# Optimization experiments

Measured on AMD Instinct MI355X. Metric: run time of the kernel, lower is better.

The kernel has to match this reference:

```python
import jax, jax.numpy as jnp
import numpy as np

N = 50000      # nodes
E = 800000     # edges (avg degree 16)
G = 512        # graphs in batch
F_IN = 14      # raw atom features
D = 64         # hidden feats_dim after projection
M = 64         # m_dim
L = 3          # egnn layers

silu = jax.nn.silu


def setup_inputs() -> dict:
    key = jax.random.key(0)
    ks = jax.random.split(key, 32)
    s = 0.1  # weight scale
    def w(k, shape):
        return jax.random.normal(k, shape, dtype=jnp.float32) * s
    inp = {
        "x": jax.random.normal(ks[0], (N, F_IN), dtype=jnp.float32),
        "pos": jax.random.normal(ks[1], (N, 3), dtype=jnp.float32),
        "edge_index": jax.random.randint(ks[2], (2, E), 0, N, dtype=jnp.int32),
        "batch": jnp.sort(jax.random.randint(ks[3], (N,), 0, G, dtype=jnp.int32)),
        # feat projection 14 -> 64
        "proj_w": w(ks[4], (F_IN, D)), "proj_b": jnp.zeros((D,), jnp.float32),
        # per-layer EGNN params, stacked over L layers
        "edge_w1": w(ks[5], (L, 2 * D, M)), "edge_b1": jnp.zeros((L, M), jnp.float32),
        "edge_w2": w(ks[6], (L, M, M)),     "edge_b2": jnp.zeros((L, M), jnp.float32),
        "node_w1": w(ks[7], (L, D + M, M)), "node_b1": jnp.zeros((L, M), jnp.float32),
        "node_w2": w(ks[8], (L, M, D)),     "node_b2": jnp.zeros((L, D), jnp.float32),
        # readout head
        "lin1_w": w(ks[9], (D, M)),  "lin1_b": jnp.zeros((M,), jnp.float32),
        "lin2_w": w(ks[10], (M, D)), "lin2_b": jnp.zeros((D,), jnp.float32),
        "lin3_w": w(ks[11], (D, M)), "lin3_b": jnp.zeros((M,), jnp.float32),
        "lin4_w": w(ks[12], (M, 1)), "lin4_b": jnp.zeros((1,), jnp.float32),
    }
    return inp


def reference(x, pos, edge_index, batch,
              proj_w, proj_b,
              edge_w1, edge_b1, edge_w2, edge_b2,
              node_w1, node_b1, node_w2, node_b2,
              lin1_w, lin1_b, lin2_w, lin2_b, lin3_w, lin3_b, lin4_w, lin4_b):
    # feature projection (do_feat_proj since dim > num_feat)
    h = x @ proj_w + proj_b                         # [N, D]
    src, dst = edge_index[0], edge_index[1]          # x_j = source, x_i = target
    for l in range(L):
        # message: edge_mlp(concat(x_i, x_j))
        cat = jnp.concatenate([h[dst], h[src]], axis=-1)       # [E, 2D]
        m = silu(cat @ edge_w1[l] + edge_b1[l])                 # [E, M]
        m = silu(m @ edge_w2[l] + edge_b2[l])                   # [E, M]
        # aggregate: scatter-add to target nodes
        agg = jax.ops.segment_sum(m, dst, num_segments=N)       # [N, M]
        # node update: node_mlp(concat(x, m_i)) + x
        u = jnp.concatenate([h, agg], axis=-1)                  # [N, D+M]
        u = silu(u @ node_w1[l] + node_b1[l])
        h = u @ node_w2[l] + node_b2[l] + h                      # residual
    per_atom_out = h                                             # [N, D]
    o = silu(h @ lin1_w + lin1_b) @ lin2_w + lin2_b              # [N, D]
    o = jax.ops.segment_sum(o, batch, num_segments=G)            # [G, D]
    o = silu(o @ lin3_w + lin3_b) @ lin4_w + lin4_b              # [G, 1]
    return o.reshape(-1), per_atom_out
```

## Files before the change

kernel.cpp:

```cpp
#include <hip/hip_runtime.h>

#define NN 50000
#define EE 800000
#define GG 512
#define LL 3

typedef short bf16x8 __attribute__((ext_vector_type(8)));
typedef float f32x4  __attribute__((ext_vector_type(4)));

__device__ __forceinline__ float silu_f(float x) {
    return x * __builtin_amdgcn_rcpf(1.0f + __expf(-x));
}
__device__ __forceinline__ unsigned short bf16_rne(float x) {
    unsigned u = __float_as_uint(x);
    u += 0x7fffu + ((u >> 16) & 1u);
    return (unsigned short)(u >> 16);
}
__device__ __forceinline__ float bflo(unsigned u) { return __uint_as_float(u << 16); }
__device__ __forceinline__ float bfhi(unsigned u) { return __uint_as_float(u & 0xffff0000u); }
__device__ __forceinline__ f32x4 mfma16(bf16x8 a, bf16x8 b, f32x4 c) {
    return __builtin_amdgcn_mfma_f32_16x16x32_bf16(a, b, c, 0, 0, 0);
}
__device__ __forceinline__ void barrier_lgkm() {
    asm volatile("s_waitcnt lgkmcnt(0)" ::: "memory");
    __builtin_amdgcn_s_barrier();
}

__global__ __launch_bounds__(256) void hist_kernel(const int* __restrict__ ei,
                                                   int* __restrict__ deg) {
    int e = blockIdx.x * 256 + threadIdx.x;
    if (e < EE) atomicAdd(&deg[ei[EE + e]], 1);
}

__global__ __launch_bounds__(512) void scanA_kernel(const int* __restrict__ deg,
                                                    int* __restrict__ rowptr,
                                                    int* __restrict__ bsum) {
    __shared__ int wsum[8];
    const int tid = threadIdx.x, b = blockIdx.x;
    int i = b * 512 + tid;
    int v = (i < NN) ? deg[i] : 0;
    int lane = tid & 63, wid = tid >> 6;
    int x = v;
#pragma unroll
    for (int s = 1; s < 64; s <<= 1) {
        int u = __shfl_up(x, s, 64);
        if (lane >= s) x += u;
    }
    if (lane == 63) wsum[wid] = x;
    __syncthreads();
    int woff = 0;
    for (int w = 0; w < wid; ++w) woff += wsum[w];
    if (i < NN) rowptr[i] = woff + x - v;
    if (tid == 511) bsum[b] = woff + x;
}

__global__ __launch_bounds__(128) void scanB_kernel(int* __restrict__ bsum, int nb) {
    __shared__ int wsum[2];
    const int tid = threadIdx.x;
    int v = (tid < nb) ? bsum[tid] : 0;
    int lane = tid & 63, wid = tid >> 6;
    int x = v;
#pragma unroll
    for (int s = 1; s < 64; s <<= 1) {
        int u = __shfl_up(x, s, 64);
        if (lane >= s) x += u;
    }
    if (lane == 63) wsum[wid] = x;
    __syncthreads();
    int woff = (wid == 1) ? wsum[0] : 0;
    if (tid < nb) bsum[tid] = woff + x - v;
}

__global__ __launch_bounds__(512) void scanC_kernel(int* __restrict__ rowptr,
                                                    int* __restrict__ cursor,
                                                    const int* __restrict__ bsum) {
    const int tid = threadIdx.x, b = blockIdx.x;
    int i = b * 512 + tid;
    if (i < NN) {
        int r = rowptr[i] + bsum[b];
        rowptr[i] = r;
        cursor[i] = r;
    }
    if (i == 0) rowptr[NN] = EE;
}

__global__ __launch_bounds__(256) void scatter_kernel(const int* __restrict__ ei,
                                                      int* __restrict__ cursor,
                                                      int* __restrict__ srcsS,
                                                      int* __restrict__ dstsS) {
    int e = blockIdx.x * 256 + threadIdx.x;
    if (e < EE) {
        int d = ei[EE + e];
        int pos = atomicAdd(&cursor[d], 1);
        srcsS[pos] = ei[e];
        dstsS[pos] = d;
    }
}

__global__ __launch_bounds__(512, 4) void pk_kernel(
    const float* __restrict__ h, const float* __restrict__ w1g,
    float* __restrict__ Pt, unsigned short* __restrict__ Pbu, int ntiles)
{
    extern __shared__ float lds[];
    float* ws = lds;
    float* hs = ws + 8192;
    const int tid = threadIdx.x;
    const int tr  = tid & 31;
    const int tc  = tid >> 5;

    for (int i = tid; i < 2048; i += 512)
        *(float4*)&ws[4 * i] = *(const float4*)&w1g[4 * i];

    for (int tile = blockIdx.x; tile < ntiles; tile += gridDim.x) {
        const int base = tile * 128;
        __syncthreads();
#pragma unroll
        for (int rep = 0; rep < 4; ++rep) {
            int idx = rep * 512 + tid;
            int r = idx >> 4, q = idx & 15;
            int n = base + r;
            float4 v = make_float4(0.f, 0.f, 0.f, 0.f);
            if (n < NN) v = *(const float4*)(h + 64 * n + 4 * q);
            *(float4*)&hs[r * 68 + 4 * q] = v;
        }
        __syncthreads();
#pragma unroll
        for (int p = 0; p < 2; ++p) {
            float acc[4][4];
#pragma unroll
            for (int jj = 0; jj < 4; ++jj)
#pragma unroll
                for (int ii = 0; ii < 4; ++ii) acc[jj][ii] = 0.f;
#pragma unroll 4
            for (int k16 = 0; k16 < 16; ++k16) {
                float4 bv0 = *(const float4*)&ws[(p * 64 + 4 * k16 + 0) * 64 + 4 * tc];
                float4 bv1 = *(const float4*)&ws[(p * 64 + 4 * k16 + 1) * 64 + 4 * tc];
                float4 bv2 = *(const float4*)&ws[(p * 64 + 4 * k16 + 2) * 64 + 4 * tc];
                float4 bv3 = *(const float4*)&ws[(p * 64 + 4 * k16 + 3) * 64 + 4 * tc];
#pragma unroll
                for (int jj = 0; jj < 4; ++jj) {
                    float4 av = *(const float4*)&hs[(tr + 32 * jj) * 68 + 4 * k16];
                    acc[jj][0] = fmaf(av.x, bv0.x, fmaf(av.y, bv1.x, fmaf(av.z, bv2.x, fmaf(av.w, bv3.x, acc[jj][0]))));
                    acc[jj][1] = fmaf(av.x, bv0.y, fmaf(av.y, bv1.y, fmaf(av.z, bv2.y, fmaf(av.w, bv3.y, acc[jj][1]))));
                    acc[jj][2] = fmaf(av.x, bv0.z, fmaf(av.y, bv1.z, fmaf(av.z, bv2.z, fmaf(av.w, bv3.z, acc[jj][2]))));
                    acc[jj][3] = fmaf(av.x, bv0.w, fmaf(av.y, bv1.w, fmaf(av.z, bv2.w, fmaf(av.w, bv3.w, acc[jj][3]))));
                }
            }
#pragma unroll
            for (int jj = 0; jj < 4; ++jj) {
                int n = base + tr + 32 * jj;
                if (n < NN) {
                    if (p == 0) {
                        *(float4*)(Pt + (size_t)64 * n + 4 * tc) =
                            make_float4(acc[jj][0], acc[jj][1], acc[jj][2], acc[jj][3]);
                    } else {
                        uint2 o;
                        o.x = ((unsigned)bf16_rne(acc[jj][1]) << 16) | bf16_rne(acc[jj][0]);
                        o.y = ((unsigned)bf16_rne(acc[jj][3]) << 16) | bf16_rne(acc[jj][2]);
                        *(uint2*)(Pbu + (size_t)64 * n + 4 * tc) = o;
                    }
                }
            }
        }
    }
}

__global__ __launch_bounds__(512, 6) void edge_kernel(
    const float* __restrict__ Pt, const unsigned short* __restrict__ Pbu,
    const int* __restrict__ srcsS, const int* __restrict__ dstsS,
    const float* __restrict__ b1g,
    const float* __restrict__ w2g, const float* __restrict__ b2g,
    unsigned short* __restrict__ m2g, int ntiles)
{
    extern __shared__ __align__(16) char smem[];
    char*  wt2s = smem;
    char*  m1s  = wt2s + 8192;
    float* b1s  = (float*)(m1s + 16384);
    float* b2s  = b1s + 64;

    const int tid = threadIdx.x;
    const int l   = tid & 63;
    const int w   = tid >> 6;
    const int mi  = w >> 1;
    const int ni  = w & 1;
    const int l15 = l & 15;
    const int l4  = l >> 4;
    const int g7  = tid & 7;

    {
        int c = tid >> 3, kc = tid & 7;
        const float* wp = w2g + (kc * 8) * 64 + c;
        bf16x8 bv;
#pragma unroll
        for (int j = 0; j < 8; ++j) bv[j] = (short)bf16_rne(wp[j * 64]);
        *(bf16x8*)(wt2s + c * 128 + ((kc * 16) ^ ((c & 7) << 4))) = bv;
    }
    if (tid < 64) { b1s[tid] = b1g[tid]; b2s[tid] = b2g[tid]; }

    int    ix_d[2], ix_s[2];
    float4 pf_a0[2], pf_a1[2];
    uint4  pf_pb[2];

    auto IDX = [&](int tt) {
        int eb = tt * 128;
#pragma unroll
        for (int it = 0; it < 2; ++it) {
            int e = (it * 512 + tid) >> 3;
            ix_d[it] = dstsS[eb + e];
            ix_s[it] = srcsS[eb + e];
        }
    };
    auto DATA = [&]() {
#pragma unroll
        for (int it = 0; it < 2; ++it) {
            const float* pt = Pt + (size_t)64 * ix_d[it] + 8 * g7;
            pf_a0[it] = *(const float4*)pt;
            pf_a1[it] = *(const float4*)(pt + 4);
            pf_pb[it] = *(const uint4*)(Pbu + (size_t)64 * ix_s[it] + 8 * g7);
        }
    };

    int tile = blockIdx.x;
    if (tile < ntiles) { IDX(tile); DATA(); }
    if (tile + gridDim.x < ntiles) IDX(tile + gridDim.x);
    barrier_lgkm();

    for (; tile < ntiles; tile += gridDim.x) {
#pragma unroll
        for (int it = 0; it < 2; ++it) {
            int e = (it * 512 + tid) >> 3;
            float4 b0  = *(const float4*)(b1s + 8 * g7);
            float4 b1v = *(const float4*)(b1s + 8 * g7 + 4);
            float v0 = silu_f(pf_a0[it].x + bflo(pf_pb[it].x) + b0.x);
            float v1 = silu_f(pf_a0[it].y + bfhi(pf_pb[it].x) + b0.y);
            float v2 = silu_f(pf_a0[it].z + bflo(pf_pb[it].y) + b0.z);
            float v3 = silu_f(pf_a0[it].w + bfhi(pf_pb[it].y) + b0.w);
            float v4 = silu_f(pf_a1[it].x + bflo(pf_pb[it].z) + b1v.x);
            float v5 = silu_f(pf_a1[it].y + bfhi(pf_pb[it].z) + b1v.y);
            float v6 = silu_f(pf_a1[it].z + bflo(pf_pb[it].w) + b1v.z);
            float v7 = silu_f(pf_a1[it].w + bfhi(pf_pb[it].w) + b1v.w);
            uint4 o;
            o.x = ((unsigned)bf16_rne(v1) << 16) | bf16_rne(v0);
            o.y = ((unsigned)bf16_rne(v3) << 16) | bf16_rne(v2);
            o.z = ((unsigned)bf16_rne(v5) << 16) | bf16_rne(v4);
            o.w = ((unsigned)bf16_rne(v7) << 16) | bf16_rne(v6);
            *(uint4*)(m1s + e * 128 + ((g7 * 16) ^ ((e & 7) << 4))) = o;
        }
        barrier_lgkm();
        int nxt = tile + gridDim.x;
        if (nxt < ntiles) {
            DATA();
            if (nxt + gridDim.x < ntiles) IDX(nxt + gridDim.x);
        }
        f32x4 acc2[2][2];
#pragma unroll
        for (int m = 0; m < 2; ++m)
#pragma unroll
            for (int n = 0; n < 2; ++n) {
                float b = b2s[32 * ni + 16 * n + l15];
                acc2[m][n] = (f32x4){b, b, b, b};
            }
        const int sw = (l15 & 7) << 4;
#pragma unroll
        for (int ks = 0; ks < 2; ++ks) {
            int kb = ks * 64 + l4 * 16;
            bf16x8 af[2], bfr[2];
#pragma unroll
            for (int m = 0; m < 2; ++m)
                af[m] = *(const bf16x8*)(m1s + (32 * mi + 16 * m + l15) * 128 + (kb ^ sw));
#pragma unroll
            for (int n = 0; n < 2; ++n)
                bfr[n] = *(const bf16x8*)(wt2s + (32 * ni + 16 * n + l15) * 128 + (kb ^ sw));
#pragma unroll
            for (int m = 0; m < 2; ++m)
#pragma unroll
                for (int n = 0; n < 2; ++n)
                    acc2[m][n] = mfma16(af[m], bfr[n], acc2[m][n]);
        }
        unsigned short* mg = m2g + (size_t)(tile * 128) * 64;
#pragma unroll
        for (int m = 0; m < 2; ++m)
#pragma unroll
            for (int n = 0; n < 2; ++n)
#pragma unroll
                for (int r = 0; r < 4; ++r) {
                    int row = 32 * mi + 16 * m + l4 * 4 + r;
                    int col = 32 * ni + 16 * n + l15;
                    mg[row * 64 + col] = bf16_rne(silu_f(acc2[m][n][r]));
                }
        barrier_lgkm();
    }
}

__global__ __launch_bounds__(256) void agg_kernel(
    const unsigned short* __restrict__ m2g, const int* __restrict__ rowptr,
    float* __restrict__ agg)
{
    int idx = blockIdx.x * 256 + threadIdx.x;
    if (idx >= NN * 16) return;
    int n = idx >> 4, c = idx & 15;
    int e0 = rowptr[n], e1 = rowptr[n + 1];
    float a0 = 0.f, a1 = 0.f, a2 = 0.f, a3 = 0.f;
    int e = e0;
    for (; e + 4 <= e1; e += 4) {
        uint2 u0 = *(const uint2*)(m2g + (size_t)(e + 0) * 64 + 4 * c);
        uint2 u1 = *(const uint2*)(m2g + (size_t)(e + 1) * 64 + 4 * c);
        uint2 u2 = *(const uint2*)(m2g + (size_t)(e + 2) * 64 + 4 * c);
        uint2 u3 = *(const uint2*)(m2g + (size_t)(e + 3) * 64 + 4 * c);
        a0 += (bflo(u0.x) + bflo(u1.x)) + (bflo(u2.x) + bflo(u3.x));
        a1 += (bfhi(u0.x) + bfhi(u1.x)) + (bfhi(u2.x) + bfhi(u3.x));
        a2 += (bflo(u0.y) + bflo(u1.y)) + (bflo(u2.y) + bflo(u3.y));
        a3 += (bfhi(u0.y) + bfhi(u1.y)) + (bfhi(u2.y) + bfhi(u3.y));
    }
    for (; e < e1; ++e) {
        uint2 u = *(const uint2*)(m2g + (size_t)e * 64 + 4 * c);
        a0 += bflo(u.x); a1 += bfhi(u.x);
        a2 += bflo(u.y); a3 += bfhi(u.y);
    }
    *(float4*)(agg + (size_t)64 * n + 4 * c) = make_float4(a0, a1, a2, a3);
}

__global__ __launch_bounds__(512, 1) void node_mlp_kernel(
    const float* __restrict__ A, const float* __restrict__ A2,
    const float* __restrict__ w1g, const float* __restrict__ b1g,
    const float* __restrict__ w2g, const float* __restrict__ b2g,
    float* __restrict__ outp, int nrows, int ntiles)
{
    extern __shared__ float lds[];
    float* ws1  = lds;
    float* ws2  = ws1 + 8192;
    float* wb1  = ws2 + 4096;
    float* wb2  = wb1 + 64;
    float* cats = wb2 + 64;
    float* m1s  = cats + 128 * 132;

    const int tid = threadIdx.x;
    const int tr  = tid & 31;
    const int tc  = tid >> 5;

    for (int i = tid; i < 2048; i += 512)
        *(float4*)&ws1[4 * i] = *(const float4*)&w1g[4 * i];
    for (int i = tid; i < 1024; i += 512)
        *(float4*)&ws2[4 * i] = *(const float4*)&w2g[4 * i];
    if (tid < 64) { wb1[tid] = b1g[tid]; wb2[tid] = b2g[tid]; }

    for (int tile = blockIdx.x; tile < ntiles; tile += gridDim.x) {
        const int base = tile * 128;
        __syncthreads();
#pragma unroll
        for (int rep = 0; rep < 8; ++rep) {
            int idx = rep * 512 + tid;
            int r = idx >> 5, q = idx & 31;
            int n = base + r;
            float4 v = make_float4(0.f, 0.f, 0.f, 0.f);
            if (n < nrows)
                v = (q < 16) ? *(const float4*)(A + 64 * n + 4 * q)
                             : *(const float4*)(A2 + 64 * n + 4 * (q - 16));
            *(float4*)&cats[r * 132 + 4 * q] = v;
        }
        __syncthreads();
        float acc[4][4];
#pragma unroll
        for (int jj = 0; jj < 4; ++jj)
#pragma unroll
            for (int ii = 0; ii < 4; ++ii) acc[jj][ii] = wb1[4 * tc + ii];
#pragma unroll 4
        for (int k16 = 0; k16 < 32; ++k16) {
            float4 bv0 = *(const float4*)&ws1[(4 * k16 + 0) * 64 + 4 * tc];
            float4 bv1 = *(const float4*)&ws1[(4 * k16 + 1) * 64 + 4 * tc];
            float4 bv2 = *(const float4*)&ws1[(4 * k16 + 2) * 64 + 4 * tc];
            float4 bv3 = *(const float4*)&ws1[(4 * k16 + 3) * 64 + 4 * tc];
#pragma unroll
            for (int jj = 0; jj < 4; ++jj) {
                float4 av = *(const float4*)&cats[(tr + 32 * jj) * 132 + 4 * k16];
                acc[jj][0] = fmaf(av.x, bv0.x, fmaf(av.y, bv1.x, fmaf(av.z, bv2.x, fmaf(av.w, bv3.x, acc[jj][0]))));
                acc[jj][1] = fmaf(av.x, bv0.y, fmaf(av.y, bv1.y, fmaf(av.z, bv2.y, fmaf(av.w, bv3.y, acc[jj][1]))));
                acc[jj][2] = fmaf(av.x, bv0.z, fmaf(av.y, bv1.z, fmaf(av.z, bv2.z, fmaf(av.w, bv3.z, acc[jj][2]))));
                acc[jj][3] = fmaf(av.x, bv0.w, fmaf(av.y, bv1.w, fmaf(av.z, bv2.w, fmaf(av.w, bv3.w, acc[jj][3]))));
            }
        }
#pragma unroll
        for (int jj = 0; jj < 4; ++jj) {
            float4 v;
            v.x = silu_f(acc[jj][0]); v.y = silu_f(acc[jj][1]);
            v.z = silu_f(acc[jj][2]); v.w = silu_f(acc[jj][3]);
            *(float4*)&m1s[(tr + 32 * jj) * 68 + 4 * tc] = v;
        }
        __syncthreads();
        float acc2[4][4];
#pragma unroll
        for (int jj = 0; jj < 4; ++jj)
#pragma unroll
            for (int ii = 0; ii < 4; ++ii) acc2[jj][ii] = wb2[4 * tc + ii];
#pragma unroll 4
        for (int k16 = 0; k16 < 16; ++k16) {
            float4 bv0 = *(const float4*)&ws2[(4 * k16 + 0) * 64 + 4 * tc];
            float4 bv1 = *(const float4*)&ws2[(4 * k16 + 1) * 64 + 4 * tc];
            float4 bv2 = *(const float4*)&ws2[(4 * k16 + 2) * 64 + 4 * tc];
            float4 bv3 = *(const float4*)&ws2[(4 * k16 + 3) * 64 + 4 * tc];
#pragma unroll
            for (int jj = 0; jj < 4; ++jj) {
                float4 av = *(const float4*)&m1s[(tr + 32 * jj) * 68 + 4 * k16];
                acc2[jj][0] = fmaf(av.x, bv0.x, fmaf(av.y, bv1.x, fmaf(av.z, bv2.x, fmaf(av.w, bv3.x, acc2[jj][0]))));
                acc2[jj][1] = fmaf(av.x, bv0.y, fmaf(av.y, bv1.y, fmaf(av.z, bv2.y, fmaf(av.w, bv3.y, acc2[jj][1]))));
                acc2[jj][2] = fmaf(av.x, bv0.z, fmaf(av.y, bv1.z, fmaf(av.z, bv2.z, fmaf(av.w, bv3.z, acc2[jj][2]))));
                acc2[jj][3] = fmaf(av.x, bv0.w, fmaf(av.y, bv1.w, fmaf(av.z, bv2.w, fmaf(av.w, bv3.w, acc2[jj][3]))));
            }
        }
#pragma unroll
        for (int jj = 0; jj < 4; ++jj) {
            int r = tr + 32 * jj;
            int n = base + r;
            if (n < nrows) {
                float4 hold = *(const float4*)&cats[r * 132 + 4 * tc];
                *(float4*)&outp[64 * n + 4 * tc] = make_float4(
                    acc2[jj][0] + hold.x, acc2[jj][1] + hold.y,
                    acc2[jj][2] + hold.z, acc2[jj][3] + hold.w);
            }
        }
    }
}

__global__ __launch_bounds__(512, 1) void rowmlp_ro_kernel(
    const float* __restrict__ A,
    const float* __restrict__ w1g, const float* __restrict__ b1g,
    const float* __restrict__ w2g, const float* __restrict__ b2g,
    const int* __restrict__ seg, float* __restrict__ outp,
    int nrows, int ntiles)
{
    extern __shared__ float lds[];
    float* ws1  = lds;
    float* ws2  = ws1 + 4096;
    float* wb1  = ws2 + 4096;
    float* wb2  = wb1 + 64;
    float* cats = wb2 + 64;
    float* m1s  = cats + 128 * 68;
    int*   segs = (int*)(m1s + 128 * 68);

    const int tid = threadIdx.x;
    const int tr  = tid & 31;
    const int tc  = tid >> 5;

    for (int i = tid; i < 1024; i += 512) {
        *(float4*)&ws1[4 * i] = *(const float4*)&w1g[4 * i];
        *(float4*)&ws2[4 * i] = *(const float4*)&w2g[4 * i];
    }
    if (tid < 64) { wb1[tid] = b1g[tid]; wb2[tid] = b2g[tid]; }

    for (int tile = blockIdx.x; tile < ntiles; tile += gridDim.x) {
        const int base = tile * 128;
        __syncthreads();
        if (tid < 128) segs[tid] = (base + tid < nrows) ? seg[base + tid] : -1;
#pragma unroll
        for (int rep = 0; rep < 4; ++rep) {
            int idx = rep * 512 + tid;
            int r = idx >> 4, q = idx & 15;
            int n = base + r;
            float4 v = make_float4(0.f, 0.f, 0.f, 0.f);
            if (n < nrows) v = *(const float4*)(A + 64 * n + 4 * q);
            *(float4*)&cats[r * 68 + 4 * q] = v;
        }
        __syncthreads();
        float acc[4][4];
#pragma unroll
        for (int jj = 0; jj < 4; ++jj)
#pragma unroll
            for (int ii = 0; ii < 4; ++ii) acc[jj][ii] = wb1[4 * tc + ii];
#pragma unroll 4
        for (int k16 = 0; k16 < 16; ++k16) {
            float4 bv0 = *(const float4*)&ws1[(4 * k16 + 0) * 64 + 4 * tc];
            float4 bv1 = *(const float4*)&ws1[(4 * k16 + 1) * 64 + 4 * tc];
            float4 bv2 = *(const float4*)&ws1[(4 * k16 + 2) * 64 + 4 * tc];
            float4 bv3 = *(const float4*)&ws1[(4 * k16 + 3) * 64 + 4 * tc];
#pragma unroll
            for (int jj = 0; jj < 4; ++jj) {
                float4 av = *(const float4*)&cats[(tr + 32 * jj) * 68 + 4 * k16];
                acc[jj][0] = fmaf(av.x, bv0.x, fmaf(av.y, bv1.x, fmaf(av.z, bv2.x, fmaf(av.w, bv3.x, acc[jj][0]))));
                acc[jj][1] = fmaf(av.x, bv0.y, fmaf(av.y, bv1.y, fmaf(av.z, bv2.y, fmaf(av.w, bv3.y, acc[jj][1]))));
                acc[jj][2] = fmaf(av.x, bv0.z, fmaf(av.y, bv1.z, fmaf(av.z, bv2.z, fmaf(av.w, bv3.z, acc[jj][2]))));
                acc[jj][3] = fmaf(av.x, bv0.w, fmaf(av.y, bv1.w, fmaf(av.z, bv2.w, fmaf(av.w, bv3.w, acc[jj][3]))));
            }
        }
#pragma unroll
        for (int jj = 0; jj < 4; ++jj) {
            float4 v;
            v.x = silu_f(acc[jj][0]); v.y = silu_f(acc[jj][1]);
            v.z = silu_f(acc[jj][2]); v.w = silu_f(acc[jj][3]);
            *(float4*)&m1s[(tr + 32 * jj) * 68 + 4 * tc] = v;
        }
        __syncthreads();
        float acc2[4][4];
#pragma unroll
        for (int jj = 0; jj < 4; ++jj)
#pragma unroll
            for (int ii = 0; ii < 4; ++ii) acc2[jj][ii] = wb2[4 * tc + ii];
#pragma unroll 4
        for (int k16 = 0; k16 < 16; ++k16) {
            float4 bv0 = *(const float4*)&ws2[(4 * k16 + 0) * 64 + 4 * tc];
            float4 bv1 = *(const float4*)&ws2[(4 * k16 + 1) * 64 + 4 * tc];
            float4 bv2 = *(const float4*)&ws2[(4 * k16 + 2) * 64 + 4 * tc];
            float4 bv3 = *(const float4*)&ws2[(4 * k16 + 3) * 64 + 4 * tc];
#pragma unroll
            for (int jj = 0; jj < 4; ++jj) {
                float4 av = *(const float4*)&m1s[(tr + 32 * jj) * 68 + 4 * k16];
                acc2[jj][0] = fmaf(av.x, bv0.x, fmaf(av.y, bv1.x, fmaf(av.z, bv2.x, fmaf(av.w, bv3.x, acc2[jj][0]))));
                acc2[jj][1] = fmaf(av.x, bv0.y, fmaf(av.y, bv1.y, fmaf(av.z, bv2.y, fmaf(av.w, bv3.y, acc2[jj][1]))));
                acc2[jj][2] = fmaf(av.x, bv0.z, fmaf(av.y, bv1.z, fmaf(av.z, bv2.z, fmaf(av.w, bv3.z, acc2[jj][2]))));
                acc2[jj][3] = fmaf(av.x, bv0.w, fmaf(av.y, bv1.w, fmaf(av.z, bv2.w, fmaf(av.w, bv3.w, acc2[jj][3]))));
            }
        }
#pragma unroll
        for (int jj = 0; jj < 4; ++jj) {
            int r = tr + 32 * jj;
            int n = base + r;
            int gid = segs[r];
            float4 vv = (n < nrows) ? make_float4(acc2[jj][0], acc2[jj][1], acc2[jj][2], acc2[jj][3])
                                    : make_float4(0.f, 0.f, 0.f, 0.f);
            unsigned f = (tr == 0 || segs[(r > 0) ? r - 1 : 0] != gid) ? 1u : 0u;
#pragma unroll
            for (int s = 1; s < 32; s <<= 1) {
                float ux = __shfl_up(vv.x, s, 32);
                float uy = __shfl_up(vv.y, s, 32);
                float uz = __shfl_up(vv.z, s, 32);
                float uw = __shfl_up(vv.w, s, 32);
                unsigned uf = __shfl_up(f, s, 32);
                if (tr >= s) {
                    if (!f) { vv.x += ux; vv.y += uy; vv.z += uz; vv.w += uw; }
                    f |= uf;
                }
            }
            bool tail = (tr == 31) || (segs[r + 1] != gid);
            if (tail && gid >= 0) {
                float* bp = outp + 64 * gid + 4 * tc;
                atomicAdd(bp + 0, vv.x); atomicAdd(bp + 1, vv.y);
                atomicAdd(bp + 2, vv.z); atomicAdd(bp + 3, vv.w);
            }
        }
    }
}

__global__ __launch_bounds__(256) void proj_kernel(
    const float* __restrict__ x, const float* __restrict__ w,
    const float* __restrict__ b, float* __restrict__ h, int n)
{
    int i = blockIdx.x * 256 + threadIdx.x;
    if (i >= n * 64) return;
    int node = i >> 6, j = i & 63;
    const float* xr = x + node * 14;
    float acc = b[j];
#pragma unroll
    for (int k = 0; k < 14; ++k) acc = fmaf(xr[k], w[k * 64 + j], acc);
    h[i] = acc;
}

__global__ __launch_bounds__(256) void head_kernel(
    const float* __restrict__ gsum,
    const float* __restrict__ w3, const float* __restrict__ b3,
    const float* __restrict__ w4, const float* __restrict__ b4,
    float* __restrict__ out, int g_count)
{
    int wid  = (blockIdx.x * 256 + threadIdx.x) >> 6;
    int lane = threadIdx.x & 63;
    if (wid >= g_count) return;
    float v = gsum[wid * 64 + lane];
    float t = b3[lane];
#pragma unroll
    for (int k = 0; k < 64; ++k) {
        float a = __shfl(v, k, 64);
        t = fmaf(a, w3[k * 64 + lane], t);
    }
    t = silu_f(t);
    float r = t * w4[lane];
#pragma unroll
    for (int off = 32; off; off >>= 1) r += __shfl_down(r, off, 64);
    if (lane == 0) out[wid] = r + b4[0];
}

extern "C" void kernel_launch(void* const* d_in, const int* in_sizes, int n_in,
                              void* d_out, int out_size, void* d_ws, size_t ws_size,
                              hipStream_t stream)
{
    const float* x      = (const float*)d_in[0];
    const int*   ei     = (const int*)d_in[2];
    const int*   batch  = (const int*)d_in[3];
    const float* proj_w = (const float*)d_in[4];
    const float* proj_b = (const float*)d_in[5];
    const float* ew1 = (const float*)d_in[6];
    const float* eb1 = (const float*)d_in[7];
    const float* ew2 = (const float*)d_in[8];
    const float* eb2 = (const float*)d_in[9];
    const float* nw1 = (const float*)d_in[10];
    const float* nb1 = (const float*)d_in[11];
    const float* nw2 = (const float*)d_in[12];
    const float* nb2 = (const float*)d_in[13];
    const float* l1w = (const float*)d_in[14]; const float* l1b = (const float*)d_in[15];
    const float* l2w = (const float*)d_in[16]; const float* l2b = (const float*)d_in[17];
    const float* l3w = (const float*)d_in[18]; const float* l3b = (const float*)d_in[19];
    const float* l4w = (const float*)d_in[20]; const float* l4b = (const float*)d_in[21];

    float* out  = (float*)d_out;
    float* h    = out + GG;

    unsigned short* m2g = (unsigned short*)d_ws;
    float* gsum = (float*)(m2g + (size_t)EE * 64);
    float* Pt   = gsum + (size_t)GG * 64;
    unsigned short* Pbu = (unsigned short*)(Pt + (size_t)NN * 64);
    int* deg    = (int*)(Pbu + (size_t)NN * 64);
    int* rowptr = deg + NN;
    int* cursor = rowptr + NN + 1;
    int* srcsS  = cursor + NN;
    int* dstsS  = srcsS + EE;
    int* bsum   = dstsS + EE;
    float* agg  = Pt;

    const size_t edge_lds = 8192 + 16384 + 256 + 256;
    const size_t pk_lds   = (size_t)(8192 + 8704) * 4;
    const size_t node_lds = (size_t)(8192 + 4096 + 128 + 128 * 132 + 128 * 68) * 4;
    const size_t ro_lds   = (size_t)(4096 + 4096 + 128 + 128 * 68 + 128 * 68) * 4 + 128 * 4;

    (void)hipFuncSetAttribute((const void*)edge_kernel,
                              hipFuncAttributeMaxDynamicSharedMemorySize, (int)edge_lds);
    (void)hipFuncSetAttribute((const void*)pk_kernel,
                              hipFuncAttributeMaxDynamicSharedMemorySize, (int)pk_lds);
    (void)hipFuncSetAttribute((const void*)node_mlp_kernel,
                              hipFuncAttributeMaxDynamicSharedMemorySize, (int)node_lds);
    (void)hipFuncSetAttribute((const void*)rowmlp_ro_kernel,
                              hipFuncAttributeMaxDynamicSharedMemorySize, (int)ro_lds);

    const int nb = (NN + 511) / 512;
    hipMemsetAsync(deg, 0, (size_t)NN * sizeof(int), stream);
    hipMemsetAsync(gsum, 0, (size_t)GG * 64 * sizeof(float), stream);
    hist_kernel<<<(EE + 255) / 256, 256, 0, stream>>>(ei, deg);
    scanA_kernel<<<nb, 512, 0, stream>>>(deg, rowptr, bsum);
    scanB_kernel<<<1, 128, 0, stream>>>(bsum, nb);
    scanC_kernel<<<nb, 512, 0, stream>>>(rowptr, cursor, bsum);
    scatter_kernel<<<(EE + 255) / 256, 256, 0, stream>>>(ei, cursor, srcsS, dstsS);

    proj_kernel<<<(NN * 64 + 255) / 256, 256, 0, stream>>>(x, proj_w, proj_b, h, NN);

    const int etiles = EE / 128;
    const int ntiles = (NN + 127) / 128;
    for (int l = 0; l < LL; ++l) {
        pk_kernel<<<ntiles, 512, pk_lds, stream>>>(h, ew1 + l * 8192, Pt, Pbu, ntiles);
        edge_kernel<<<1024, 512, edge_lds, stream>>>(
            Pt, Pbu, srcsS, dstsS, eb1 + l * 64, ew2 + l * 4096, eb2 + l * 64,
            m2g, etiles);
        agg_kernel<<<(NN * 16 + 255) / 256, 256, 0, stream>>>(m2g, rowptr, agg);
        node_mlp_kernel<<<196, 512, node_lds, stream>>>(
            h, agg, nw1 + l * 8192, nb1 + l * 64, nw2 + l * 4096, nb2 + l * 64,
            h, NN, ntiles);
    }
    rowmlp_ro_kernel<<<196, 512, ro_lds, stream>>>(
        h, l1w, l1b, l2w, l2b, batch, gsum, NN, ntiles);
    head_kernel<<<GG / 4, 256, 0, stream>>>(gsum, l3w, l3b, l4w, l4b, out, GG);
}
```

Before: 511.3 us.

## Fuse segment-sum aggregation into edge kernel via LDS segmented reduction

```diff
diff --git a/kernel.cpp b/kernel.cpp
--- a/kernel.cpp
+++ b/kernel.cpp
@@ -165,18 +165,20 @@
     }
 }
 
-__global__ __launch_bounds__(512, 6) void edge_kernel(
+__global__ __launch_bounds__(512, 4) void edge_kernel(
     const float* __restrict__ Pt, const unsigned short* __restrict__ Pbu,
     const int* __restrict__ srcsS, const int* __restrict__ dstsS,
     const float* __restrict__ b1g,
     const float* __restrict__ w2g, const float* __restrict__ b2g,
-    unsigned short* __restrict__ m2g, int ntiles)
+    float* __restrict__ agg, int ntiles)
 {
     extern __shared__ __align__(16) char smem[];
-    char*  wt2s = smem;
-    char*  m1s  = wt2s + 8192;
-    float* b1s  = (float*)(m1s + 16384);
-    float* b2s  = b1s + 64;
+    char*  wt2s  = smem;
+    char*  m1s   = wt2s + 8192;
+    char*  m2h   = m1s + 16384;
+    float* b1s   = (float*)(m2h + 17408);
+    float* b2s   = b1s + 64;
+    int*   dstsL = (int*)(b2s + 64);
 
     const int tid = threadIdx.x;
     const int l   = tid & 63;
@@ -197,9 +199,10 @@
     }
     if (tid < 64) { b1s[tid] = b1g[tid]; b2s[tid] = b2g[tid]; }
 
-    int    ix_d[2], ix_s[2];
+    int    ix_d[2], ix_s[2], ix_pd = 0;
     float4 pf_a0[2], pf_a1[2];
     uint4  pf_pb[2];
+    int    pf_d = 0;
 
     auto IDX = [&](int tt) {
         int eb = tt * 128;
@@ -209,6 +212,7 @@
             ix_d[it] = dstsS[eb + e];
             ix_s[it] = srcsS[eb + e];
         }
+        ix_pd = (tid < 128) ? dstsS[eb + tid] : 0;
     };
     auto DATA = [&]() {
 #pragma unroll
@@ -218,14 +222,17 @@
             pf_a1[it] = *(const float4*)(pt + 4);
             pf_pb[it] = *(const uint4*)(Pbu + (size_t)64 * ix_s[it] + 8 * g7);
         }
+        pf_d = ix_pd;
     };
 
     int tile = blockIdx.x;
+    int buf  = 0;
     if (tile < ntiles) { IDX(tile); DATA(); }
     if (tile + gridDim.x < ntiles) IDX(tile + gridDim.x);
     barrier_lgkm();
 
     for (; tile < ntiles; tile += gridDim.x) {
+        if (tid < 128) dstsL[buf * 128 + tid] = pf_d;
 #pragma unroll
         for (int it = 0; it < 2; ++it) {
             int e = (it * 512 + tid) >> 3;
@@ -277,7 +284,6 @@
                 for (int n = 0; n < 2; ++n)
                     acc2[m][n] = mfma16(af[m], bfr[n], acc2[m][n]);
         }
-        unsigned short* mg = m2g + (size_t)(tile * 128) * 64;
 #pragma unroll
         for (int m = 0; m < 2; ++m)
 #pragma unroll
@@ -286,38 +292,51 @@
                 for (int r = 0; r < 4; ++r) {
                     int row = 32 * mi + 16 * m + l4 * 4 + r;
                     int col = 32 * ni + 16 * n + l15;
-                    mg[row * 64 + col] = bf16_rne(silu_f(acc2[m][n][r]));
+                    *(unsigned short*)(m2h + row * 136 + col * 2) =
+                        bf16_rne(silu_f(acc2[m][n][r]));
                 }
         barrier_lgkm();
-    }
-}
-
-__global__ __launch_bounds__(256) void agg_kernel(
-    const unsigned short* __restrict__ m2g, const int* __restrict__ rowptr,
-    float* __restrict__ agg)
-{
-    int idx = blockIdx.x * 256 + threadIdx.x;
-    if (idx >= NN * 16) return;
-    int n = idx >> 4, c = idx & 15;
-    int e0 = rowptr[n], e1 = rowptr[n + 1];
-    float a0 = 0.f, a1 = 0.f, a2 = 0.f, a3 = 0.f;
-    int e = e0;
-    for (; e + 4 <= e1; e += 4) {
-        uint2 u0 = *(const uint2*)(m2g + (size_t)(e + 0) * 64 + 4 * c);
-        uint2 u1 = *(const uint2*)(m2g + (size_t)(e + 1) * 64 + 4 * c);
-        uint2 u2 = *(const uint2*)(m2g + (size_t)(e + 2) * 64 + 4 * c);
-        uint2 u3 = *(const uint2*)(m2g + (size_t)(e + 3) * 64 + 4 * c);
-        a0 += (bflo(u0.x) + bflo(u1.x)) + (bflo(u2.x) + bflo(u3.x));
-        a1 += (bfhi(u0.x) + bfhi(u1.x)) + (bfhi(u2.x) + bfhi(u3.x));
-        a2 += (bflo(u0.y) + bflo(u1.y)) + (bflo(u2.y) + bflo(u3.y));
-        a3 += (bfhi(u0.y) + bfhi(u1.y)) + (bfhi(u2.y) + bfhi(u3.y));
-    }
-    for (; e < e1; ++e) {
-        uint2 u = *(const uint2*)(m2g + (size_t)e * 64 + 4 * c);
-        a0 += bflo(u.x); a1 += bfhi(u.x);
-        a2 += bflo(u.y); a3 += bfhi(u.y);
-    }
-    *(float4*)(agg + (size_t)64 * n + 4 * c) = make_float4(a0, a1, a2, a3);
+        {
+            const int* dL = dstsL + buf * 128;
+            int r  = tid & 127;
+            int cg = tid >> 7;
+            int d  = dL[r];
+            bool head = (r == 0) || (dL[r - 1] != d);
+            if (head) {
+                float s[16];
+#pragma unroll
+                for (int j = 0; j < 16; ++j) s[j] = 0.f;
+                int rr = r;
+                do {
+                    const char* p = m2h + rr * 136 + cg * 32;
+                    uint2 u0 = *(const uint2*)(p);
+                    uint2 u1 = *(const uint2*)(p + 8);
+                    uint2 u2 = *(const uint2*)(p + 16);
+                    uint2 u3 = *(const uint2*)(p + 24);
+                    s[0]  += bflo(u0.x); s[1]  += bfhi(u0.x);
+                    s[2]  += bflo(u0.y); s[3]  += bfhi(u0.y);
+                    s[4]  += bflo(u1.x); s[5]  += bfhi(u1.x);
+                    s[6]  += bflo(u1.y); s[7]  += bfhi(u1.y);
+                    s[8]  += bflo(u2.x); s[9]  += bfhi(u2.x);
+                    s[10] += bflo(u2.y); s[11] += bfhi(u2.y);
+                    s[12] += bflo(u3.x); s[13] += bfhi(u3.x);
+                    s[14] += bflo(u3.y); s[15] += bfhi(u3.y);
+                    ++rr;
+                } while (rr < 128 && dL[rr] == d);
+                float* ap = agg + (size_t)64 * d + cg * 16;
+                if (r > 0 && rr < 128) {
+                    *(float4*)(ap + 0)  = make_float4(s[0], s[1], s[2], s[3]);
+                    *(float4*)(ap + 4)  = make_float4(s[4], s[5], s[6], s[7]);
+                    *(float4*)(ap + 8)  = make_float4(s[8], s[9], s[10], s[11]);
+                    *(float4*)(ap + 12) = make_float4(s[12], s[13], s[14], s[15]);
+                } else {
+#pragma unroll
+                    for (int j = 0; j < 16; ++j) atomicAdd(ap + j, s[j]);
+                }
+            }
+        }
+        buf ^= 1;
+    }
 }
 
 __global__ __launch_bounds__(512, 1) void node_mlp_kernel(
@@ -601,8 +620,8 @@
     float* out  = (float*)d_out;
     float* h    = out + GG;
 
-    unsigned short* m2g = (unsigned short*)d_ws;
-    float* gsum = (float*)(m2g + (size_t)EE * 64);
+    float* agg  = (float*)d_ws;
+    float* gsum = agg + (size_t)NN * 64;
     float* Pt   = gsum + (size_t)GG * 64;
     unsigned short* Pbu = (unsigned short*)(Pt + (size_t)NN * 64);
     int* deg    = (int*)(Pbu + (size_t)NN * 64);
@@ -611,9 +630,8 @@
     int* srcsS  = cursor + NN;
     int* dstsS  = srcsS + EE;
     int* bsum   = dstsS + EE;
-    float* agg  = Pt;
-
-    const size_t edge_lds = 8192 + 16384 + 256 + 256;
+
+    const size_t edge_lds = 8192 + 16384 + 17408 + 256 + 256 + 1024;
     const size_t pk_lds   = (size_t)(8192 + 8704) * 4;
     const size_t node_lds = (size_t)(8192 + 4096 + 128 + 128 * 132 + 128 * 68) * 4;
     const size_t ro_lds   = (size_t)(4096 + 4096 + 128 + 128 * 68 + 128 * 68) * 4 + 128 * 4;
@@ -642,10 +660,10 @@
     const int ntiles = (NN + 127) / 128;
     for (int l = 0; l < LL; ++l) {
         pk_kernel<<<ntiles, 512, pk_lds, stream>>>(h, ew1 + l * 8192, Pt, Pbu, ntiles);
-        edge_kernel<<<1024, 512, edge_lds, stream>>>(
+        hipMemsetAsync(agg, 0, (size_t)NN * 64 * sizeof(float), stream);
+        edge_kernel<<<768, 512, edge_lds, stream>>>(
             Pt, Pbu, srcsS, dstsS, eb1 + l * 64, ew2 + l * 4096, eb2 + l * 64,
-            m2g, etiles);
-        agg_kernel<<<(NN * 16 + 255) / 256, 256, 0, stream>>>(m2g, rowptr, agg);
+            agg, etiles);
         node_mlp_kernel<<<196, 512, node_lds, stream>>>(
             h, agg, nw1 + l * 8192, nb1 + l * 64, nw2 + l * 4096, nb2 + l * 64,
             h, NN, ntiles);
```

Result: slower. 719.3 us (+40.7%).

## Rewrite per-node projection kernel with bf16 MFMA and swizzled LDS tiles

Applied to the files above, without the earlier changes.

```diff
diff --git a/kernel.cpp b/kernel.cpp
--- a/kernel.cpp
+++ b/kernel.cpp
@@ -97,69 +97,135 @@
     }
 }
 
-__global__ __launch_bounds__(512, 4) void pk_kernel(
+__global__ __launch_bounds__(512, 2) void pk_kernel(
     const float* __restrict__ h, const float* __restrict__ w1g,
     float* __restrict__ Pt, unsigned short* __restrict__ Pbu, int ntiles)
 {
-    extern __shared__ float lds[];
-    float* ws = lds;
-    float* hs = ws + 8192;
+    extern __shared__ __align__(16) char smem[];
+    char*  hb = smem;
+    char*  wt = hb + 16384;
+    float* tp = (float*)(wt + 16384);
+
     const int tid = threadIdx.x;
-    const int tr  = tid & 31;
-    const int tc  = tid >> 5;
-
-    for (int i = tid; i < 2048; i += 512)
-        *(float4*)&ws[4 * i] = *(const float4*)&w1g[4 * i];
+    const int l   = tid & 63;
+    const int w   = tid >> 6;
+    const int mi  = w >> 1;
+    const int ni  = w & 1;
+    const int l15 = l & 15;
+    const int l4  = l >> 4;
+    const int sw  = (l15 & 7) << 4;
+
+    {
+        int c = tid >> 2, kq0 = tid & 3;
+#pragma unroll
+        for (int hf = 0; hf < 2; ++hf) {
+            int kq = kq0 + 4 * hf;
+            const float* wp = w1g + (size_t)((c >> 6) * 64 + kq * 8) * 64 + (c & 63);
+            bf16x8 bv;
+#pragma unroll
+            for (int j = 0; j < 8; ++j) bv[j] = (short)bf16_rne(wp[j * 64]);
+            *(bf16x8*)(wt + c * 128 + ((kq * 16) ^ ((c & 7) << 4))) = bv;
+        }
+    }
 
     for (int tile = blockIdx.x; tile < ntiles; tile += gridDim.x) {
         const int base = tile * 128;
         __syncthreads();
-#pragma unroll
-        for (int rep = 0; rep < 4; ++rep) {
-            int idx = rep * 512 + tid;
-            int r = idx >> 4, q = idx & 15;
+        {
+            int r = tid >> 2, q = tid & 3;
             int n = base + r;
-            float4 v = make_float4(0.f, 0.f, 0.f, 0.f);
-            if (n < NN) v = *(const float4*)(h + 64 * n + 4 * q);
-            *(float4*)&hs[r * 68 + 4 * q] = v;
-        }
-        __syncthreads();
-#pragma unroll
-        for (int p = 0; p < 2; ++p) {
-            float acc[4][4];
-#pragma unroll
-            for (int jj = 0; jj < 4; ++jj)
-#pragma unroll
-                for (int ii = 0; ii < 4; ++ii) acc[jj][ii] = 0.f;
-#pragma unroll 4
-            for (int k16 = 0; k16 < 16; ++k16) {
-                float4 bv0 = *(const float4*)&ws[(p * 64 + 4 * k16 + 0) * 64 + 4 * tc];
-                float4 bv1 = *(const float4*)&ws[(p * 64 + 4 * k16 + 1) * 64 + 4 * tc];
-                float4 bv2 = *(const float4*)&ws[(p * 64 + 4 * k16 + 2) * 64 + 4 * tc];
-                float4 bv3 = *(const float4*)&ws[(p * 64 + 4 * k16 + 3) * 64 + 4 * tc];
-#pragma unroll
-                for (int jj = 0; jj < 4; ++jj) {
-                    float4 av = *(const float4*)&hs[(tr + 32 * jj) * 68 + 4 * k16];
-                    acc[jj][0] = fmaf(av.x, bv0.x, fmaf(av.y, bv1.x, fmaf(av.z, bv2.x, fmaf(av.w, bv3.x, acc[jj][0]))));
-                    acc[jj][1] = fmaf(av.x, bv0.y, fmaf(av.y, bv1.y, fmaf(av.z, bv2.y, fmaf(av.w, bv3.y, acc[jj][1]))));
-                    acc[jj][2] = fmaf(av.x, bv0.z, fmaf(av.y, bv1.z, fmaf(av.z, bv2.z, fmaf(av.w, bv3.z, acc[jj][2]))));
-                    acc[jj][3] = fmaf(av.x, bv0.w, fmaf(av.y, bv1.w, fmaf(av.z, bv2.w, fmaf(av.w, bv3.w, acc[jj][3]))));
+            float v[16];
+#pragma unroll
+            for (int j = 0; j < 16; ++j) v[j] = 0.f;
+            if (n < NN) {
+                const float* hp = h + (size_t)64 * n + q * 16;
+#pragma unroll
+                for (int j = 0; j < 4; ++j) {
+                    float4 t = *(const float4*)(hp + 4 * j);
+                    v[4 * j] = t.x; v[4 * j + 1] = t.y;
+                    v[4 * j + 2] = t.z; v[4 * j + 3] = t.w;
                 }
             }
-#pragma unroll
-            for (int jj = 0; jj < 4; ++jj) {
-                int n = base + tr + 32 * jj;
-                if (n < NN) {
-                    if (p == 0) {
-                        *(float4*)(Pt + (size_t)64 * n + 4 * tc) =
-                            make_float4(acc[jj][0], acc[jj][1], acc[jj][2], acc[jj][3]);
-                    } else {
-                        uint2 o;
-                        o.x = ((unsigned)bf16_rne(acc[jj][1]) << 16) | bf16_rne(acc[jj][0]);
-                        o.y = ((unsigned)bf16_rne(acc[jj][3]) << 16) | bf16_rne(acc[jj][2]);
-                        *(uint2*)(Pbu + (size_t)64 * n + 4 * tc) = o;
-                    }
+            bf16x8 b0, b1;
+#pragma unroll
+            for (int j = 0; j < 8; ++j) {
+                b0[j] = (short)bf16_rne(v[j]);
+                b1[j] = (short)bf16_rne(v[8 + j]);
+            }
+            int swr = (r & 7) << 4;
+            *(bf16x8*)(hb + r * 128 + ((q * 32) ^ swr))      = b0;
+            *(bf16x8*)(hb + r * 128 + ((q * 32 + 16) ^ swr)) = b1;
+        }
+        __syncthreads();
+        f32x4 acc[2][4];
+#pragma unroll
+        for (int m = 0; m < 2; ++m)
+#pragma unroll
+            for (int n = 0; n < 4; ++n) acc[m][n] = (f32x4){0.f, 0.f, 0.f, 0.f};
+#pragma unroll
+        for (int ks = 0; ks < 2; ++ks) {
+            int kb = ks * 64 + l4 * 16;
+            bf16x8 af[2], bf[4];
+#pragma unroll
+            for (int m = 0; m < 2; ++m)
+                af[m] = *(const bf16x8*)(hb + (32 * mi + 16 * m + l15) * 128 + (kb ^ sw));
+#pragma unroll
+            for (int n = 0; n < 4; ++n)
+                bf[n] = *(const bf16x8*)(wt + (64 * ni + 16 * n + l15) * 128 + (kb ^ sw));
+#pragma unroll
+            for (int m = 0; m < 2; ++m)
+#pragma unroll
+                for (int n = 0; n < 4; ++n)
+                    acc[m][n] = mfma16(af[m], bf[n], acc[m][n]);
+        }
+        __syncthreads();
+        if (ni == 0) {
+#pragma unroll
+            for (int m = 0; m < 2; ++m)
+#pragma unroll
+                for (int n = 0; n < 4; ++n)
+#pragma unroll
+                    for (int r = 0; r < 4; ++r)
+                        tp[(32 * mi + 16 * m + l4 * 4 + r) * 68 + 16 * n + l15] =
+                            acc[m][n][r];
+        }
+        __syncthreads();
+        {
+            int r = tid >> 2, q = tid & 3;
+            int n = base + r;
+            if (n < NN) {
+                float* op = Pt + (size_t)64 * n + q * 16;
+#pragma unroll
+                for (int j = 0; j < 4; ++j)
+                    *(float4*)(op + 4 * j) = *(const float4*)&tp[r * 68 + q * 16 + 4 * j];
+            }
+        }
+        __syncthreads();
+        if (ni == 1) {
+#pragma unroll
+            for (int m = 0; m < 2; ++m)
+#pragma unroll
+                for (int n = 0; n < 4; ++n)
+#pragma unroll
+                    for (int r = 0; r < 4; ++r)
+                        tp[(32 * mi + 16 * m + l4 * 4 + r) * 68 + 16 * n + l15] =
+                            acc[m][n][r];
+        }
+        __syncthreads();
+        {
+            int r = tid >> 2, q = tid & 3;
+            int n = base + r;
+            if (n < NN) {
+                unsigned uu[8];
+#pragma unroll
+                for (int j = 0; j < 8; ++j) {
+                    float lo = tp[r * 68 + q * 16 + 2 * j];
+                    float hi = tp[r * 68 + q * 16 + 2 * j + 1];
+                    uu[j] = ((unsigned)bf16_rne(hi) << 16) | bf16_rne(lo);
                 }
+                uint4* op = (uint4*)(Pbu + (size_t)64 * n + q * 16);
+                op[0] = make_uint4(uu[0], uu[1], uu[2], uu[3]);
+                op[1] = make_uint4(uu[4], uu[5], uu[6], uu[7]);
             }
         }
     }
@@ -614,7 +680,7 @@
     float* agg  = Pt;
 
     const size_t edge_lds = 8192 + 16384 + 256 + 256;
-    const size_t pk_lds   = (size_t)(8192 + 8704) * 4;
+    const size_t pk_lds   = 16384 + 16384 + 34816;
     const size_t node_lds = (size_t)(8192 + 4096 + 128 + 128 * 132 + 128 * 68) * 4;
     const size_t ro_lds   = (size_t)(4096 + 4096 + 128 + 128 * 68 + 128 * 68) * 4 + 128 * 4;
 
```

New measurement: 485.9 us. 1.05x faster.
